# Optimization experiments

Measured on AMD Instinct MI355X. Metric: run time of the kernel, lower is better.

Reference implementation:

```python
import jax, jax.numpy as jnp
import numpy as np

N_EMB = 1024
N_HEADS = 16
HS = N_EMB // N_HEADS  # 64
BASE = 10000.0


def _rope_cache(T):
    # theta uses dim = n_emb (as in the source), sliced to hs//2 frequencies
    i = jnp.arange(HS // 2, dtype=jnp.float32)
    theta = BASE ** (-2.0 * i / N_EMB)            # [hs/2]
    pos = jnp.arange(T, dtype=jnp.float32)        # [T]
    ang = pos[:, None] * theta[None, :]           # [T, hs/2]
    return jnp.cos(ang), jnp.sin(ang)


def _apply_rope(x, cos, sin):
    # x: [B, T, nh, hs]; rotate consecutive pairs along hs
    b, t, nh, hs = x.shape
    xr = x.reshape(b, t, nh, hs // 2, 2)
    c = cos[None, :, None, :]
    s = sin[None, :, None, :]
    r0 = xr[..., 0] * c - xr[..., 1] * s
    r1 = xr[..., 1] * c + xr[..., 0] * s
    return jnp.stack([r0, r1], axis=-1).reshape(b, t, nh, hs)


def setup_inputs() -> dict:
    key = jax.random.key(0)
    k1, k2, k3, k4 = jax.random.split(key, 4)
    B, T = 2, 2048
    w_std = 0.02
    x = jax.random.normal(k1, (B, T, N_EMB), jnp.float32)
    Wq = jax.random.normal(k2, (N_EMB, N_EMB), jnp.float32) * w_std
    Wk = jax.random.normal(k3, (N_EMB, N_EMB), jnp.float32) * w_std
    Wv = jax.random.normal(k4, (N_EMB, N_EMB), jnp.float32) * w_std
    return {"x": x, "Wq": Wq, "Wk": Wk, "Wv": Wv}


def reference(x, Wq, Wk, Wv):
    B, T, C = x.shape
    # nn.Linear(bias=False): y = x @ W.T
    q = (x @ Wq.T).reshape(B, T, N_HEADS, HS)
    k = (x @ Wk.T).reshape(B, T, N_HEADS, HS)
    v = (x @ Wv.T).reshape(B, T, N_HEADS, HS)
    cos, sin = _rope_cache(T)
    q = _apply_rope(q, cos, sin)
    k = _apply_rope(k, cos, sin)
    # scale uses C (n_emb), as in the source (not head_size)
    wei = jnp.einsum('bqhd,bkhd->bhqk', q, k) * (C ** -0.5)  # [B, nh, T, T]
    mask = jnp.tril(jnp.ones((T, T), dtype=bool))
    wei = jnp.where(mask[None, None], wei, -jnp.inf)
    wei = jax.nn.softmax(wei, axis=-1)
    # dropout is identity in eval mode
    out = jnp.einsum('bhqk,bkhd->bqhd', wei, v).reshape(B, T, C)
    return out
```

## Files before the change

kernel.cpp:

```cpp
#include <hip/hip_runtime.h>
#include <stdint.h>

typedef unsigned short u16;
typedef __bf16 bf16x8 __attribute__((ext_vector_type(8)));
typedef unsigned short u16x8 __attribute__((ext_vector_type(8)));
typedef float f32x4 __attribute__((ext_vector_type(4)));

#define LOG2E 1.4426950408889634f

typedef const __attribute__((address_space(1))) uint32_t as1_u32;
typedef __attribute__((address_space(3))) uint32_t as3_u32;

__device__ __forceinline__ u16 f2bf(float f) {
  union { float f; uint32_t i; } v; v.f = f;
  uint32_t r = (v.i + 0x7fffu + ((v.i >> 16) & 1u)) >> 16;
  return (u16)r;
}
__device__ __forceinline__ float bf2f(u16 u) {
  union { uint32_t i; float f; } v; v.i = ((uint32_t)u) << 16; return v.f;
}

__device__ __forceinline__ void gld_lds16(const void* g, void* l) {
  as1_u32* gp = (as1_u32*)((uintptr_t)g);
  as3_u32* lp = (as3_u32*)(uint32_t)(uintptr_t)(l);
  __builtin_amdgcn_global_load_lds(gp, lp, 16, 0, 0);
}

__global__ __launch_bounds__(256) void f32_to_bf16(
    const float* __restrict__ x, const float* __restrict__ wq,
    const float* __restrict__ wk, const float* __restrict__ wv,
    u16* __restrict__ xc, u16* __restrict__ wqc,
    u16* __restrict__ wkc, u16* __restrict__ wvc) {
  const int z = blockIdx.y;
  const float* src = z == 0 ? x : (z == 1 ? wq : (z == 2 ? wk : wv));
  u16* dst = z == 0 ? xc : (z == 1 ? wqc : (z == 2 ? wkc : wvc));
  const int n = z == 0 ? (1 << 22) : (1 << 20);

  const int idx = (blockIdx.x * 256 + (int)threadIdx.x) * 8;
  if (idx >= n) return;
  const f32x4 a = *(const f32x4*)&src[idx];
  const f32x4 b = *(const f32x4*)&src[idx + 4];
  u16x8 o;
#pragma unroll
  for (int j = 0; j < 4; j++) { o[j] = f2bf(a[j]); o[j + 4] = f2bf(b[j]); }
  *(u16x8*)&dst[idx] = o;
}

__global__ __launch_bounds__(256) void qkv_gemm(
    const u16* __restrict__ xc, const u16* __restrict__ wqc,
    const u16* __restrict__ wkc, const u16* __restrict__ wvc,
    u16* __restrict__ qo, u16* __restrict__ ko, u16* __restrict__ vt) {
  __shared__ __align__(16) u16 As[128 * 32];
  __shared__ __align__(16) u16 Bs[128 * 32];

  const int tid = threadIdx.x;
  const int lane = tid & 63;
  const int w = tid >> 6;
  const int wm = w >> 1, wn = w & 1;
  const int quad = lane >> 4, m16 = lane & 15;
  const int which = blockIdx.z;

  const u16* __restrict__ Ap;
  const u16* __restrict__ Bp;
  int m0, n0;
  if (which == 2) {
    Ap = wvc; Bp = xc;
    m0 = blockIdx.x * 128;
    n0 = blockIdx.y * 128;
  } else {
    Ap = xc; Bp = which == 0 ? wqc : wkc;
    m0 = blockIdx.y * 128;
    n0 = blockIdx.x * 128;
  }

  const f32x4 z4 = {0.f, 0.f, 0.f, 0.f};
  f32x4 acc[4][4];
#pragma unroll
  for (int i = 0; i < 4; i++)
#pragma unroll
    for (int j = 0; j < 4; j++) acc[i][j] = z4;

  const int rowA = m0 + w * 32 + (lane >> 2);
  const int rowB = n0 + w * 32 + (lane >> 2);
  const int cch = (lane & 3) * 8;

  for (int k0 = 0; k0 < 1024; k0 += 32) {
    __syncthreads();
#pragma unroll
    for (int i = 0; i < 2; i++) {
      gld_lds16(&Ap[(size_t)(rowA + i * 16) * 1024 + k0 + cch],
                &As[(w * 32 + i * 16) * 32]);
      gld_lds16(&Bp[(size_t)(rowB + i * 16) * 1024 + k0 + cch],
                &Bs[(w * 32 + i * 16) * 32]);
    }
    __syncthreads();

    bf16x8 af[4], bfr[4];
#pragma unroll
    for (int t = 0; t < 4; t++) {
      af[t]  = *(const bf16x8*)&As[(wm * 64 + t * 16 + m16) * 32 + quad * 8];
      bfr[t] = *(const bf16x8*)&Bs[(wn * 64 + t * 16 + m16) * 32 + quad * 8];
    }
#pragma unroll
    for (int mt = 0; mt < 4; mt++)
#pragma unroll
      for (int nt = 0; nt < 4; nt++)
        acc[mt][nt] = __builtin_amdgcn_mfma_f32_16x16x32_bf16(
            af[mt], bfr[nt], acc[mt][nt], 0, 0, 0);
  }

  if (which < 2) {
    u16* __restrict__ out = which == 0 ? qo : ko;
#pragma unroll
    for (int mt = 0; mt < 4; mt++) {
      const int row = m0 + wm * 64 + mt * 16 + quad * 4;
#pragma unroll
      for (int nt = 0; nt < 4; nt++) {
        const int n = n0 + wn * 64 + nt * 16 + m16;
        f32x4 a = acc[mt][nt];
#pragma unroll
        for (int r = 0; r < 4; r++)
          out[(size_t)(row + r) * 1024 + n] = f2bf(a[r]);
      }
    }
  } else {
#pragma unroll
    for (int mt = 0; mt < 4; mt++) {
      const int row = m0 + wm * 64 + mt * 16 + quad * 4;
#pragma unroll
      for (int nt = 0; nt < 4; nt++) {
        const int n = n0 + wn * 64 + nt * 16 + m16;
        f32x4 a = acc[mt][nt];
#pragma unroll
        for (int r = 0; r < 4; r++)
          vt[(size_t)(row + r) * 4096 + n] = f2bf(a[r]);
      }
    }
  }
}

__global__ __launch_bounds__(256) void rope_inplace(u16* __restrict__ qb,
                                                    u16* __restrict__ kb) {
  u16* buf = blockIdx.y == 0 ? qb : kb;
  const int p = blockIdx.x * 256 + (int)threadIdx.x;
  const int nidx = p * 2;
  const int row = nidx >> 10;
  const int col = nidx & 1023;
  const int i = (col & 63) >> 1;
  const int t = row & 2047;
  const float theta = exp2f(-(float)i * 0.02595256324130752f);
  const float ang = (float)t * theta;
  float s, c;
  sincosf(ang, &s, &c);
  const float a0 = bf2f(buf[(size_t)row * 1024 + col]);
  const float a1 = bf2f(buf[(size_t)row * 1024 + col + 1]);
  buf[(size_t)row * 1024 + col]     = f2bf(a0 * c - a1 * s);
  buf[(size_t)row * 1024 + col + 1] = f2bf(a1 * c + a0 * s);
}

__global__ __launch_bounds__(256) void flash_attn(
    const u16* __restrict__ qg, const u16* __restrict__ kg,
    const u16* __restrict__ vt, float* __restrict__ out) {
  __shared__ __align__(16) u16 Qs[64 * 72];
  __shared__ __align__(16) u16 Ks[64 * 72];
  __shared__ __align__(16) u16 Vs[64 * 72];
  __shared__ __align__(16) u16 Ps[64 * 72];

  const int tid = threadIdx.x, lane = tid & 63, w = tid >> 6;
  const int quad = lane >> 4, m16 = lane & 15;
  const int h = blockIdx.y, b = blockIdx.z;
  const size_t base = (size_t)b * 2048 * 1024 + (size_t)h * 64;
  const size_t vbase = (size_t)(h * 64) * 4096 + (size_t)b * 2048;
  const float SC = 0.03125f * LOG2E;

  const f32x4 z4 = {0.f, 0.f, 0.f, 0.f};
  const int srow = tid >> 2, sc = (tid & 3) * 16;

  for (int pass = 0; pass < 2; ++pass) {
    const int qt = pass == 0 ? (int)blockIdx.x : 31 - (int)blockIdx.x;
    const int q0 = qt * 64;

    __syncthreads();
    {
      const u16* src = &qg[base + (size_t)(q0 + srow) * 1024 + sc];
      *(u16x8*)&Qs[srow * 72 + sc] = *(const u16x8*)src;
      *(u16x8*)&Qs[srow * 72 + sc + 8] = *(const u16x8*)(src + 8);
    }
    u16x8 kr0, kr1, vr0, vr1;
    {
      const u16* ks = &kg[base + (size_t)srow * 1024 + sc];
      kr0 = *(const u16x8*)ks; kr1 = *(const u16x8*)(ks + 8);
      const u16* vs = &vt[vbase + (size_t)srow * 4096 + sc];
      vr0 = *(const u16x8*)vs; vr1 = *(const u16x8*)(vs + 8);
    }
    __syncthreads();
    const bf16x8 qf0 = *(const bf16x8*)&Qs[(w * 16 + m16) * 72 + quad * 8];
    const bf16x8 qf1 = *(const bf16x8*)&Qs[(w * 16 + m16) * 72 + 32 + quad * 8];

    float l_p[4] = {0.f, 0.f, 0.f, 0.f};
    f32x4 O[4];
#pragma unroll
    for (int d = 0; d < 4; d++) O[d] = z4;

    const int qrow0 = q0 + w * 16 + quad * 4;

    for (int kt = 0; kt <= qt; ++kt) {
      const int k0 = kt * 64;
      if (kt) __syncthreads();
      *(u16x8*)&Ks[srow * 72 + sc] = kr0;
      *(u16x8*)&Ks[srow * 72 + sc + 8] = kr1;
      *(u16x8*)&Vs[srow * 72 + sc] = vr0;
      *(u16x8*)&Vs[srow * 72 + sc + 8] = vr1;
      __syncthreads();
      if (kt < qt) {
        const u16* ks = &kg[base + (size_t)(k0 + 64 + srow) * 1024 + sc];
        kr0 = *(const u16x8*)ks; kr1 = *(const u16x8*)(ks + 8);
        const u16* vs = &vt[vbase + (size_t)srow * 4096 + k0 + 64 + sc];
        vr0 = *(const u16x8*)vs; vr1 = *(const u16x8*)(vs + 8);
      }

      f32x4 S[4];
#pragma unroll
      for (int nt = 0; nt < 4; nt++) {
        const bf16x8 kf0 = *(const bf16x8*)&Ks[(nt * 16 + m16) * 72 + quad * 8];
        const bf16x8 kf1 =
            *(const bf16x8*)&Ks[(nt * 16 + m16) * 72 + 32 + quad * 8];
        S[nt] = __builtin_amdgcn_mfma_f32_16x16x32_bf16(qf0, kf0, z4, 0, 0, 0);
        S[nt] = __builtin_amdgcn_mfma_f32_16x16x32_bf16(qf1, kf1, S[nt], 0, 0, 0);
      }

      const bool diag = (kt == qt);
#pragma unroll
      for (int nt = 0; nt < 4; nt++) {
        const int key = k0 + nt * 16 + m16;
#pragma unroll
        for (int r = 0; r < 4; r++) {
          float p = exp2f(S[nt][r] * SC);
          if (diag && key > qrow0 + r) p = 0.f;
          union { float f; uint32_t i; } u; u.f = p;
          const uint32_t hi = u.i & 0xffff0000u;
          Ps[(w * 16 + quad * 4 + r) * 72 + nt * 16 + m16] = (u16)(hi >> 16);
          union { uint32_t i; float f; } pr; pr.i = hi;
          l_p[r] += pr.f;
        }
      }

      const bf16x8 pf0 = *(const bf16x8*)&Ps[(w * 16 + m16) * 72 + quad * 8];
      const bf16x8 pf1 =
          *(const bf16x8*)&Ps[(w * 16 + m16) * 72 + 32 + quad * 8];
#pragma unroll
      for (int dt = 0; dt < 4; dt++) {
        const bf16x8 vf0 = *(const bf16x8*)&Vs[(dt * 16 + m16) * 72 + quad * 8];
        const bf16x8 vf1 =
            *(const bf16x8*)&Vs[(dt * 16 + m16) * 72 + 32 + quad * 8];
        O[dt] = __builtin_amdgcn_mfma_f32_16x16x32_bf16(pf0, vf0, O[dt], 0, 0, 0);
        O[dt] = __builtin_amdgcn_mfma_f32_16x16x32_bf16(pf1, vf1, O[dt], 0, 0, 0);
      }
    }

#pragma unroll
    for (int off = 1; off < 16; off <<= 1)
#pragma unroll
      for (int r = 0; r < 4; r++) l_p[r] += __shfl_xor(l_p[r], off);
    float inv[4];
#pragma unroll
    for (int r = 0; r < 4; r++) inv[r] = 1.0f / l_p[r];

#pragma unroll
    for (int dt = 0; dt < 4; dt++)
#pragma unroll
      for (int r = 0; r < 4; r++)
        out[base + (size_t)(qrow0 + r) * 1024 + dt * 16 + m16] =
            O[dt][r] * inv[r];
  }
}

extern "C" void kernel_launch(void* const* d_in, const int* in_sizes, int n_in,
                              void* d_out, int out_size, void* d_ws, size_t ws_size,
                              hipStream_t stream) {
  const float* x  = (const float*)d_in[0];
  const float* Wq = (const float*)d_in[1];
  const float* Wk = (const float*)d_in[2];
  const float* Wv = (const float*)d_in[3];
  u16* qb  = (u16*)d_ws;
  u16* kb  = qb  + (size_t)4096 * 1024;
  u16* vtw = kb  + (size_t)4096 * 1024;
  u16* xc  = vtw + (size_t)4096 * 1024;
  u16* wqc = xc  + (size_t)4096 * 1024;
  u16* wkc = wqc + (size_t)1024 * 1024;
  u16* wvc = wkc + (size_t)1024 * 1024;

  f32_to_bf16<<<dim3(2048, 4), 256, 0, stream>>>(x, Wq, Wk, Wv,
                                                 xc, wqc, wkc, wvc);
  qkv_gemm<<<dim3(8, 32, 3), 256, 0, stream>>>(xc, wqc, wkc, wvc,
                                               qb, kb, vtw);
  rope_inplace<<<dim3(8192, 2), 256, 0, stream>>>(qb, kb);
  flash_attn<<<dim3(16, 16, 2), 256, 0, stream>>>(qb, kb, vtw, (float*)d_out);
}
```

Before: 171.8 us.

## Split KV tiles across two wave groups and fuse Q RoPE into attention

The attention kernel now runs 512 threads as two groups of four waves. Each group handles alternating 64-key tiles, with both tiles staged together into double-sized LDS buffers, and the partial O and row sums are merged through shared memory at the end. RoPE for Q is applied in registers when Q fragments are loaded, so the separate rope pass now only touches K. This adds parallelism per query tile and removes one global read/write pass over Q, at the cost of a shared-memory reduction, more LDS, and extra sincos work per block.

```diff
diff --git a/kernel.cpp b/kernel.cpp
--- a/kernel.cpp
+++ b/kernel.cpp
@@ -139,9 +139,7 @@
   }
 }
 
-__global__ __launch_bounds__(256) void rope_inplace(u16* __restrict__ qb,
-                                                    u16* __restrict__ kb) {
-  u16* buf = blockIdx.y == 0 ? qb : kb;
+__global__ __launch_bounds__(256) void rope_inplace_k(u16* __restrict__ kb) {
   const int p = blockIdx.x * 256 + (int)threadIdx.x;
   const int nidx = p * 2;
   const int row = nidx >> 10;
@@ -152,126 +150,193 @@
   const float ang = (float)t * theta;
   float s, c;
   sincosf(ang, &s, &c);
-  const float a0 = bf2f(buf[(size_t)row * 1024 + col]);
-  const float a1 = bf2f(buf[(size_t)row * 1024 + col + 1]);
-  buf[(size_t)row * 1024 + col]     = f2bf(a0 * c - a1 * s);
-  buf[(size_t)row * 1024 + col + 1] = f2bf(a1 * c + a0 * s);
-}
-
-__global__ __launch_bounds__(256) void flash_attn(
+  const float a0 = bf2f(kb[(size_t)row * 1024 + col]);
+  const float a1 = bf2f(kb[(size_t)row * 1024 + col + 1]);
+  kb[(size_t)row * 1024 + col]     = f2bf(a0 * c - a1 * s);
+  kb[(size_t)row * 1024 + col + 1] = f2bf(a1 * c + a0 * s);
+}
+
+__global__ __launch_bounds__(512) void flash_attn(
     const u16* __restrict__ qg, const u16* __restrict__ kg,
     const u16* __restrict__ vt, float* __restrict__ out) {
-  __shared__ __align__(16) u16 Qs[64 * 72];
-  __shared__ __align__(16) u16 Ks[64 * 72];
-  __shared__ __align__(16) u16 Vs[64 * 72];
-  __shared__ __align__(16) u16 Ps[64 * 72];
+  __shared__ __align__(16) u16 Ks[2 * 64 * 72];
+  __shared__ __align__(16) u16 Vs[2 * 64 * 72];
+  __shared__ __align__(16) u16 Ps[2 * 64 * 72];
 
   const int tid = threadIdx.x, lane = tid & 63, w = tid >> 6;
+  const int grp = w >> 2, wl = w & 3;
   const int quad = lane >> 4, m16 = lane & 15;
   const int h = blockIdx.y, b = blockIdx.z;
   const size_t base = (size_t)b * 2048 * 1024 + (size_t)h * 64;
   const size_t vbase = (size_t)(h * 64) * 4096 + (size_t)b * 2048;
   const float SC = 0.03125f * LOG2E;
-
   const f32x4 z4 = {0.f, 0.f, 0.f, 0.f};
-  const int srow = tid >> 2, sc = (tid & 3) * 16;
+
+  const int sarr = tid >> 7;
+  const int su = tid & 127;
+  const int sr = su >> 1, sh = (su & 1) * 32;
+  const int stileoff = sarr >> 1;
+  const bool skrole = (sarr & 1) == 0;
+  u16* const sdst = (sarr == 0) ? &Ks[0] : (sarr == 1) ? &Vs[0]
+                  : (sarr == 2) ? &Ks[64 * 72] : &Vs[64 * 72];
+
+  const int lbase = grp * (64 * 72);
 
   for (int pass = 0; pass < 2; ++pass) {
     const int qt = pass == 0 ? (int)blockIdx.x : 31 - (int)blockIdx.x;
     const int q0 = qt * 64;
 
-    __syncthreads();
+    const int trow = q0 + wl * 16 + m16;
+    bf16x8 qf[2];
     {
-      const u16* src = &qg[base + (size_t)(q0 + srow) * 1024 + sc];
-      *(u16x8*)&Qs[srow * 72 + sc] = *(const u16x8*)src;
-      *(u16x8*)&Qs[srow * 72 + sc + 8] = *(const u16x8*)(src + 8);
-    }
-    u16x8 kr0, kr1, vr0, vr1;
+      const u16* qp = &qg[base + (size_t)trow * 1024 + quad * 8];
+      u16x8 qraw[2];
+      qraw[0] = *(const u16x8*)qp;
+      qraw[1] = *(const u16x8*)(qp + 32);
+#pragma unroll
+      for (int f = 0; f < 2; f++) {
+        u16x8 o;
+#pragma unroll
+        for (int p = 0; p < 4; p++) {
+          const float a0 = bf2f(qraw[f][2 * p]);
+          const float a1 = bf2f(qraw[f][2 * p + 1]);
+          const int i = f * 16 + quad * 4 + p;
+          const float th = exp2f(-(float)i * 0.02595256324130752f);
+          float s, c;
+          sincosf((float)trow * th, &s, &c);
+          o[2 * p]     = f2bf(a0 * c - a1 * s);
+          o[2 * p + 1] = f2bf(a1 * c + a0 * s);
+        }
+        qf[f] = *(bf16x8*)&o;
+      }
+    }
+
+    u16x8 pr[4];
     {
-      const u16* ks = &kg[base + (size_t)srow * 1024 + sc];
-      kr0 = *(const u16x8*)ks; kr1 = *(const u16x8*)(ks + 8);
-      const u16* vs = &vt[vbase + (size_t)srow * 4096 + sc];
-      vr0 = *(const u16x8*)vs; vr1 = *(const u16x8*)(vs + 8);
-    }
-    __syncthreads();
-    const bf16x8 qf0 = *(const bf16x8*)&Qs[(w * 16 + m16) * 72 + quad * 8];
-    const bf16x8 qf1 = *(const bf16x8*)&Qs[(w * 16 + m16) * 72 + 32 + quad * 8];
+      const int tile = stileoff;
+      if (tile <= qt) {
+        if (skrole) {
+          const u16* s = &kg[base + (size_t)(tile * 64 + sr) * 1024 + sh];
+#pragma unroll
+          for (int j = 0; j < 4; j++) pr[j] = *(const u16x8*)(s + j * 8);
+        } else {
+          const u16* s = &vt[vbase + (size_t)sr * 4096 + tile * 64 + sh];
+#pragma unroll
+          for (int j = 0; j < 4; j++) pr[j] = *(const u16x8*)(s + j * 8);
+        }
+      }
+    }
 
     float l_p[4] = {0.f, 0.f, 0.f, 0.f};
     f32x4 O[4];
 #pragma unroll
     for (int d = 0; d < 4; d++) O[d] = z4;
 
-    const int qrow0 = q0 + w * 16 + quad * 4;
-
-    for (int kt = 0; kt <= qt; ++kt) {
-      const int k0 = kt * 64;
-      if (kt) __syncthreads();
-      *(u16x8*)&Ks[srow * 72 + sc] = kr0;
-      *(u16x8*)&Ks[srow * 72 + sc + 8] = kr1;
-      *(u16x8*)&Vs[srow * 72 + sc] = vr0;
-      *(u16x8*)&Vs[srow * 72 + sc + 8] = vr1;
+    const int qrow0 = q0 + wl * 16 + quad * 4;
+
+    for (int kt0 = 0; kt0 <= qt; kt0 += 2) {
       __syncthreads();
-      if (kt < qt) {
-        const u16* ks = &kg[base + (size_t)(k0 + 64 + srow) * 1024 + sc];
-        kr0 = *(const u16x8*)ks; kr1 = *(const u16x8*)(ks + 8);
-        const u16* vs = &vt[vbase + (size_t)srow * 4096 + k0 + 64 + sc];
-        vr0 = *(const u16x8*)vs; vr1 = *(const u16x8*)(vs + 8);
-      }
-
-      f32x4 S[4];
-#pragma unroll
-      for (int nt = 0; nt < 4; nt++) {
-        const bf16x8 kf0 = *(const bf16x8*)&Ks[(nt * 16 + m16) * 72 + quad * 8];
-        const bf16x8 kf1 =
-            *(const bf16x8*)&Ks[(nt * 16 + m16) * 72 + 32 + quad * 8];
-        S[nt] = __builtin_amdgcn_mfma_f32_16x16x32_bf16(qf0, kf0, z4, 0, 0, 0);
-        S[nt] = __builtin_amdgcn_mfma_f32_16x16x32_bf16(qf1, kf1, S[nt], 0, 0, 0);
-      }
-
-      const bool diag = (kt == qt);
-#pragma unroll
-      for (int nt = 0; nt < 4; nt++) {
-        const int key = k0 + nt * 16 + m16;
+#pragma unroll
+      for (int j = 0; j < 4; j++)
+        *(u16x8*)&sdst[sr * 72 + sh + j * 8] = pr[j];
+      __syncthreads();
+
+      {
+        const int tile = kt0 + 2 + stileoff;
+        if (tile <= qt) {
+          if (skrole) {
+            const u16* s = &kg[base + (size_t)(tile * 64 + sr) * 1024 + sh];
+#pragma unroll
+            for (int j = 0; j < 4; j++) pr[j] = *(const u16x8*)(s + j * 8);
+          } else {
+            const u16* s = &vt[vbase + (size_t)sr * 4096 + tile * 64 + sh];
+#pragma unroll
+            for (int j = 0; j < 4; j++) pr[j] = *(const u16x8*)(s + j * 8);
+          }
+        }
+      }
+
+      const int ktg = kt0 + grp;
+      if (ktg <= qt) {
+        const int k0 = ktg * 64;
+
+        f32x4 S[4];
+#pragma unroll
+        for (int nt = 0; nt < 4; nt++) {
+          const bf16x8 kf0 =
+              *(const bf16x8*)&Ks[lbase + (nt * 16 + m16) * 72 + quad * 8];
+          const bf16x8 kf1 =
+              *(const bf16x8*)&Ks[lbase + (nt * 16 + m16) * 72 + 32 + quad * 8];
+          S[nt] = __builtin_amdgcn_mfma_f32_16x16x32_bf16(qf[0], kf0, z4, 0, 0, 0);
+          S[nt] = __builtin_amdgcn_mfma_f32_16x16x32_bf16(qf[1], kf1, S[nt], 0, 0, 0);
+        }
+
+        const bool diag = (ktg == qt);
+#pragma unroll
+        for (int nt = 0; nt < 4; nt++) {
+          const int key = k0 + nt * 16 + m16;
+#pragma unroll
+          for (int r = 0; r < 4; r++) {
+            float p = exp2f(S[nt][r] * SC);
+            if (diag && key > qrow0 + r) p = 0.f;
+            union { float f; uint32_t i; } u; u.f = p;
+            const uint32_t hi = u.i & 0xffff0000u;
+            Ps[lbase + (wl * 16 + quad * 4 + r) * 72 + nt * 16 + m16] =
+                (u16)(hi >> 16);
+            union { uint32_t i; float f; } pf_; pf_.i = hi;
+            l_p[r] += pf_.f;
+          }
+        }
+
+        const bf16x8 pf0 =
+            *(const bf16x8*)&Ps[lbase + (wl * 16 + m16) * 72 + quad * 8];
+        const bf16x8 pf1 =
+            *(const bf16x8*)&Ps[lbase + (wl * 16 + m16) * 72 + 32 + quad * 8];
+#pragma unroll
+        for (int dt = 0; dt < 4; dt++) {
+          const bf16x8 vf0 =
+              *(const bf16x8*)&Vs[lbase + (dt * 16 + m16) * 72 + quad * 8];
+          const bf16x8 vf1 =
+              *(const bf16x8*)&Vs[lbase + (dt * 16 + m16) * 72 + 32 + quad * 8];
+          O[dt] = __builtin_amdgcn_mfma_f32_16x16x32_bf16(pf0, vf0, O[dt], 0, 0, 0);
+          O[dt] = __builtin_amdgcn_mfma_f32_16x16x32_bf16(pf1, vf1, O[dt], 0, 0, 0);
+        }
+      }
+    }
+
+#pragma unroll
+    for (int off = 1; off < 16; off <<= 1)
+#pragma unroll
+      for (int r = 0; r < 4; r++) l_p[r] += __shfl_xor(l_p[r], off);
+
+    __syncthreads();
+    float* const Osh = (float*)Ks;
+    float* const Lsh = (float*)Vs;
+    if (grp == 1) {
+#pragma unroll
+      for (int dt = 0; dt < 4; dt++)
+#pragma unroll
+        for (int r = 0; r < 4; r++)
+          Osh[(wl * 16 + quad * 4 + r) * 65 + dt * 16 + m16] = O[dt][r];
+#pragma unroll
+      for (int r = 0; r < 4; r++)
+        Lsh[wl * 16 + quad * 4 + r] = l_p[r];
+    }
+    __syncthreads();
+    if (grp == 0) {
+      float inv[4];
+#pragma unroll
+      for (int r = 0; r < 4; r++)
+        inv[r] = 1.0f / (l_p[r] + Lsh[wl * 16 + quad * 4 + r]);
+#pragma unroll
+      for (int dt = 0; dt < 4; dt++)
 #pragma unroll
         for (int r = 0; r < 4; r++) {
-          float p = exp2f(S[nt][r] * SC);
-          if (diag && key > qrow0 + r) p = 0.f;
-          union { float f; uint32_t i; } u; u.f = p;
-          const uint32_t hi = u.i & 0xffff0000u;
-          Ps[(w * 16 + quad * 4 + r) * 72 + nt * 16 + m16] = (u16)(hi >> 16);
-          union { uint32_t i; float f; } pr; pr.i = hi;
-          l_p[r] += pr.f;
-        }
-      }
-
-      const bf16x8 pf0 = *(const bf16x8*)&Ps[(w * 16 + m16) * 72 + quad * 8];
-      const bf16x8 pf1 =
-          *(const bf16x8*)&Ps[(w * 16 + m16) * 72 + 32 + quad * 8];
-#pragma unroll
-      for (int dt = 0; dt < 4; dt++) {
-        const bf16x8 vf0 = *(const bf16x8*)&Vs[(dt * 16 + m16) * 72 + quad * 8];
-        const bf16x8 vf1 =
-            *(const bf16x8*)&Vs[(dt * 16 + m16) * 72 + 32 + quad * 8];
-        O[dt] = __builtin_amdgcn_mfma_f32_16x16x32_bf16(pf0, vf0, O[dt], 0, 0, 0);
-        O[dt] = __builtin_amdgcn_mfma_f32_16x16x32_bf16(pf1, vf1, O[dt], 0, 0, 0);
-      }
-    }
-
-#pragma unroll
-    for (int off = 1; off < 16; off <<= 1)
-#pragma unroll
-      for (int r = 0; r < 4; r++) l_p[r] += __shfl_xor(l_p[r], off);
-    float inv[4];
-#pragma unroll
-    for (int r = 0; r < 4; r++) inv[r] = 1.0f / l_p[r];
-
-#pragma unroll
-    for (int dt = 0; dt < 4; dt++)
-#pragma unroll
-      for (int r = 0; r < 4; r++)
-        out[base + (size_t)(qrow0 + r) * 1024 + dt * 16 + m16] =
-            O[dt][r] * inv[r];
+          const float o =
+              O[dt][r] + Osh[(wl * 16 + quad * 4 + r) * 65 + dt * 16 + m16];
+          out[base + (size_t)(qrow0 + r) * 1024 + dt * 16 + m16] = o * inv[r];
+        }
+    }
   }
 }
 
@@ -294,6 +359,6 @@
                                                  xc, wqc, wkc, wvc);
   qkv_gemm<<<dim3(8, 32, 3), 256, 0, stream>>>(xc, wqc, wkc, wvc,
                                                qb, kb, vtw);
-  rope_inplace<<<dim3(8192, 2), 256, 0, stream>>>(qb, kb);
-  flash_attn<<<dim3(16, 16, 2), 256, 0, stream>>>(qb, kb, vtw, (float*)d_out);
-}
+  rope_inplace_k<<<dim3(8192), 256, 0, stream>>>(kb);
+  flash_attn<<<dim3(16, 16, 2), 512, 0, stream>>>(qb, kb, vtw, (float*)d_out);
+}
```

Measured after the change: 175.7 us. 2.2% more time.

## Fuse fp32-to-bf16 conversion into QKV GEMM with register-prefetched tile loads

Applied to the files above, without the earlier changes.

Removes the standalone conversion kernel and its bf16 workspace copies. The QKV GEMM now reads fp32 x and weights directly, converts them to bf16 in registers and writes them into LDS. It also prefetches the next k-tile into registers while the current tile is consumed. The aim is to drop one launch and the write/re-read of converted tensors, at the cost of the GEMM reading twice the bytes per tile, repeatedly across blocks, and losing the direct global-to-LDS loads.

```diff
diff --git a/kernel.cpp b/kernel.cpp
--- a/kernel.cpp
+++ b/kernel.cpp
@@ -8,9 +8,6 @@
 
 #define LOG2E 1.4426950408889634f
 
-typedef const __attribute__((address_space(1))) uint32_t as1_u32;
-typedef __attribute__((address_space(3))) uint32_t as3_u32;
-
 __device__ __forceinline__ u16 f2bf(float f) {
   union { float f; uint32_t i; } v; v.f = f;
   uint32_t r = (v.i + 0x7fffu + ((v.i >> 16) & 1u)) >> 16;
@@ -20,35 +17,9 @@
   union { uint32_t i; float f; } v; v.i = ((uint32_t)u) << 16; return v.f;
 }
 
-__device__ __forceinline__ void gld_lds16(const void* g, void* l) {
-  as1_u32* gp = (as1_u32*)((uintptr_t)g);
-  as3_u32* lp = (as3_u32*)(uint32_t)(uintptr_t)(l);
-  __builtin_amdgcn_global_load_lds(gp, lp, 16, 0, 0);
-}
-
-__global__ __launch_bounds__(256) void f32_to_bf16(
+__global__ __launch_bounds__(256) void qkv_gemm(
     const float* __restrict__ x, const float* __restrict__ wq,
     const float* __restrict__ wk, const float* __restrict__ wv,
-    u16* __restrict__ xc, u16* __restrict__ wqc,
-    u16* __restrict__ wkc, u16* __restrict__ wvc) {
-  const int z = blockIdx.y;
-  const float* src = z == 0 ? x : (z == 1 ? wq : (z == 2 ? wk : wv));
-  u16* dst = z == 0 ? xc : (z == 1 ? wqc : (z == 2 ? wkc : wvc));
-  const int n = z == 0 ? (1 << 22) : (1 << 20);
-
-  const int idx = (blockIdx.x * 256 + (int)threadIdx.x) * 8;
-  if (idx >= n) return;
-  const f32x4 a = *(const f32x4*)&src[idx];
-  const f32x4 b = *(const f32x4*)&src[idx + 4];
-  u16x8 o;
-#pragma unroll
-  for (int j = 0; j < 4; j++) { o[j] = f2bf(a[j]); o[j + 4] = f2bf(b[j]); }
-  *(u16x8*)&dst[idx] = o;
-}
-
-__global__ __launch_bounds__(256) void qkv_gemm(
-    const u16* __restrict__ xc, const u16* __restrict__ wqc,
-    const u16* __restrict__ wkc, const u16* __restrict__ wvc,
     u16* __restrict__ qo, u16* __restrict__ ko, u16* __restrict__ vt) {
   __shared__ __align__(16) u16 As[128 * 32];
   __shared__ __align__(16) u16 Bs[128 * 32];
@@ -60,15 +31,15 @@
   const int quad = lane >> 4, m16 = lane & 15;
   const int which = blockIdx.z;
 
-  const u16* __restrict__ Ap;
-  const u16* __restrict__ Bp;
+  const float* __restrict__ Ap;
+  const float* __restrict__ Bp;
   int m0, n0;
   if (which == 2) {
-    Ap = wvc; Bp = xc;
+    Ap = wv; Bp = x;
     m0 = blockIdx.x * 128;
     n0 = blockIdx.y * 128;
   } else {
-    Ap = xc; Bp = which == 0 ? wqc : wkc;
+    Ap = x; Bp = which == 0 ? wq : wk;
     m0 = blockIdx.y * 128;
     n0 = blockIdx.x * 128;
   }
@@ -84,16 +55,38 @@
   const int rowB = n0 + w * 32 + (lane >> 2);
   const int cch = (lane & 3) * 8;
 
+  f32x4 ra[2][2], rb[2][2];
+#pragma unroll
+  for (int i = 0; i < 2; i++) {
+    const float* pa = &Ap[(size_t)(rowA + i * 16) * 1024 + cch];
+    const float* pb = &Bp[(size_t)(rowB + i * 16) * 1024 + cch];
+    ra[i][0] = *(const f32x4*)pa; ra[i][1] = *(const f32x4*)(pa + 4);
+    rb[i][0] = *(const f32x4*)pb; rb[i][1] = *(const f32x4*)(pb + 4);
+  }
+
   for (int k0 = 0; k0 < 1024; k0 += 32) {
     __syncthreads();
 #pragma unroll
     for (int i = 0; i < 2; i++) {
-      gld_lds16(&Ap[(size_t)(rowA + i * 16) * 1024 + k0 + cch],
-                &As[(w * 32 + i * 16) * 32]);
-      gld_lds16(&Bp[(size_t)(rowB + i * 16) * 1024 + k0 + cch],
-                &Bs[(w * 32 + i * 16) * 32]);
-    }
-    __syncthreads();
+      u16x8 ca, cb;
+#pragma unroll
+      for (int j = 0; j < 4; j++) {
+        ca[j] = f2bf(ra[i][0][j]); ca[j + 4] = f2bf(ra[i][1][j]);
+        cb[j] = f2bf(rb[i][0][j]); cb[j + 4] = f2bf(rb[i][1][j]);
+      }
+      *(u16x8*)&As[(w * 32 + i * 16) * 32 + lane * 8] = ca;
+      *(u16x8*)&Bs[(w * 32 + i * 16) * 32 + lane * 8] = cb;
+    }
+    __syncthreads();
+    if (k0 + 32 < 1024) {
+#pragma unroll
+      for (int i = 0; i < 2; i++) {
+        const float* pa = &Ap[(size_t)(rowA + i * 16) * 1024 + k0 + 32 + cch];
+        const float* pb = &Bp[(size_t)(rowB + i * 16) * 1024 + k0 + 32 + cch];
+        ra[i][0] = *(const f32x4*)pa; ra[i][1] = *(const f32x4*)(pa + 4);
+        rb[i][0] = *(const f32x4*)pb; rb[i][1] = *(const f32x4*)(pb + 4);
+      }
+    }
 
     bf16x8 af[4], bfr[4];
 #pragma unroll
@@ -285,15 +278,8 @@
   u16* qb  = (u16*)d_ws;
   u16* kb  = qb  + (size_t)4096 * 1024;
   u16* vtw = kb  + (size_t)4096 * 1024;
-  u16* xc  = vtw + (size_t)4096 * 1024;
-  u16* wqc = xc  + (size_t)4096 * 1024;
-  u16* wkc = wqc + (size_t)1024 * 1024;
-  u16* wvc = wkc + (size_t)1024 * 1024;
-
-  f32_to_bf16<<<dim3(2048, 4), 256, 0, stream>>>(x, Wq, Wk, Wv,
-                                                 xc, wqc, wkc, wvc);
-  qkv_gemm<<<dim3(8, 32, 3), 256, 0, stream>>>(xc, wqc, wkc, wvc,
-                                               qb, kb, vtw);
+
+  qkv_gemm<<<dim3(8, 32, 3), 256, 0, stream>>>(x, Wq, Wk, Wv, qb, kb, vtw);
   rope_inplace<<<dim3(8192, 2), 256, 0, stream>>>(qb, kb);
   flash_attn<<<dim3(16, 16, 2), 256, 0, stream>>>(qb, kb, vtw, (float*)d_out);
 }
```

Result: slower. 177.0 us (+3.0%).
